# Kernel optimization log

Hardware: AMD Instinct MI355X
Metric: run time of the kernel (lower is better)

Reference implementation:

```python
import jax, jax.numpy as jnp
import numpy as np

H, HKV, D = 8, 1, 256  # query heads, kv heads, head_dim (Gemma-2B-like)


def apply_rope(x, sin, cos):
    # x: [B, h, D, S]; sin/cos: [B, 1, D//2, S]
    x1, x2 = jnp.split(x, 2, axis=-2)
    return jnp.concatenate((x1 * cos - x2 * sin, x2 * cos + x1 * sin), axis=-2)


def setup_inputs() -> dict:
    key = jax.random.key(0)
    ks = jax.random.split(key, 12)
    B, hidden, S = 2, 2048, 2048
    half = D // 2
    Xq = jax.random.normal(ks[0], (B, hidden, S), jnp.float32)
    Xkv = jax.random.normal(ks[1], (B, hidden, S), jnp.float32)
    sin_q = jax.random.uniform(ks[2], (B, 1, half, S), jnp.float32, -1.0, 1.0)
    cos_q = jax.random.uniform(ks[3], (B, 1, half, S), jnp.float32, -1.0, 1.0)
    sin_k = jax.random.uniform(ks[4], (B, 1, half, S), jnp.float32, -1.0, 1.0)
    cos_k = jax.random.uniform(ks[5], (B, 1, half, S), jnp.float32, -1.0, 1.0)
    attn_mask = jnp.zeros((B, 1, S, S), jnp.float32)
    scale = 0.02
    Wq = jax.random.normal(ks[6], (H * D, hidden), jnp.float32) * scale
    Wk = jax.random.normal(ks[7], (HKV * D, hidden), jnp.float32) * scale
    Wv = jax.random.normal(ks[8], (HKV * D, hidden), jnp.float32) * scale
    Wo = jax.random.normal(ks[9], (hidden, H * D), jnp.float32) * scale
    return {"Xq": Xq, "Xkv": Xkv, "sin_q": sin_q, "cos_q": cos_q,
            "sin_k": sin_k, "cos_k": cos_k, "attn_mask": attn_mask,
            "Wq": Wq, "Wk": Wk, "Wv": Wv, "Wo": Wo}


def reference(Xq, Xkv, sin_q, cos_q, sin_k, cos_k, attn_mask, Wq, Wk, Wv, Wo):
    B, hidden, Sq = Xq.shape
    Sk = Xkv.shape[-1]
    # ANEDenseGeneral = 1x1 conv over channels-first layout
    q = jnp.einsum('oc,bcs->bos', Wq, Xq).reshape(B, H, D, Sq)
    q = apply_rope(q, sin_q, cos_q)
    k = jnp.einsum('oc,bcs->bos', Wk, Xkv).reshape(B, HKV, D, Sk)
    k = apply_rope(k, sin_k, cos_k)
    v = jnp.einsum('oc,bcs->bos', Wv, Xkv).reshape(B, HKV, D, Sk)
    # GQA: broadcast kv heads to query heads
    rep = H // HKV
    k = jnp.repeat(k, rep, axis=1)
    v = jnp.repeat(v, rep, axis=1)
    scale = 1.0 / jnp.sqrt(jnp.asarray(D, Xq.dtype))
    scores = jnp.einsum('bhdq,bhdk->bhqk', q, k) * scale + attn_mask
    probs = jax.nn.softmax(scores, axis=-1)
    out = jnp.einsum('bhqk,bhdk->bhdq', probs, v).reshape(B, H * D, Sq)
    return jnp.einsum('oc,bcs->bos', Wo, out).astype(Xq.dtype)
```

## Files before the change

### kernel.cpp

```cpp
#include <hip/hip_runtime.h>

typedef __bf16 bf16;
typedef __bf16 bf16x8 __attribute__((ext_vector_type(8)));
typedef __bf16 bf16x4 __attribute__((ext_vector_type(4)));
typedef float f32x4 __attribute__((ext_vector_type(4)));

static constexpr int Hh = 8;
static constexpr int Dd = 256;
static constexpr int Ss = 2048;
static constexpr int Cc = 2048;
static constexpr int NS = 4096;

typedef const __attribute__((address_space(1))) unsigned int as1_u32;
typedef __attribute__((address_space(3))) unsigned int as3_u32;

__device__ __forceinline__ void gl_lds16(const void* g, void* l) {
  __builtin_amdgcn_global_load_lds((as1_u32*)(unsigned long long)g,
                                   (as3_u32*)(unsigned int)(unsigned long long)l,
                                   16, 0, 0);
}

__device__ __forceinline__ f32x4 mfma16(bf16x8 a, bf16x8 b, f32x4 c) {
  return __builtin_amdgcn_mfma_f32_16x16x32_bf16(a, b, c, 0, 0, 0);
}

__global__ __launch_bounds__(256) void cvt_all(
    const float* __restrict__ Wq, const float* __restrict__ Wo,
    const float* __restrict__ Wk, const float* __restrict__ Wv,
    bf16* __restrict__ Wq_bf, bf16* __restrict__ Wo_bf,
    bf16* __restrict__ Wkv_bf) {
  const int blk = blockIdx.x;
  const float* in;
  bf16* out;
  int base;
  if (blk < 4096) {
    in = Wq; out = Wq_bf; base = blk;
  } else if (blk < 8192) {
    in = Wo; out = Wo_bf; base = blk - 4096;
  } else if (blk < 8704) {
    in = Wk; out = Wkv_bf; base = blk - 8192;
  } else {
    in = Wv; out = Wkv_bf + (long)Dd * Cc; base = blk - 8704;
  }
  int i = (base * 256 + threadIdx.x) * 4;
  const float4 v = *(const float4*)(in + i);
  bf16x4 o;
  o[0] = (bf16)v.x; o[1] = (bf16)v.y; o[2] = (bf16)v.z; o[3] = (bf16)v.w;
  *(bf16x4*)(out + i) = o;
}

__global__ __launch_bounds__(256) void transpose_cvt(const float* __restrict__ in,
                                                     bf16* __restrict__ out,
                                                     int R, int S) {
  __shared__ float t[32][33];
  const int b = blockIdx.z;
  const long base = (long)b * R * S;
  const int s0 = blockIdx.x * 32, r0 = blockIdx.y * 32;
  const int tx = threadIdx.x, ty = threadIdx.y;
#pragma unroll
  for (int i = 0; i < 32; i += 8)
    t[ty + i][tx] = in[base + (long)(r0 + ty + i) * S + s0 + tx];
  __syncthreads();
#pragma unroll
  for (int i = 0; i < 32; i += 8)
    out[base + (long)(s0 + ty + i) * R + r0 + tx] = (bf16)t[tx][ty + i];
}

__global__ __launch_bounds__(256) void transpose_cvt4(
    const float* __restrict__ s0, const float* __restrict__ s1,
    const float* __restrict__ s2, const float* __restrict__ s3,
    bf16* __restrict__ d0, bf16* __restrict__ d1, bf16* __restrict__ d2,
    bf16* __restrict__ d3, int R, int S) {
  __shared__ float t[32][33];
  const int arr = blockIdx.y >> 2;
  const int r0 = (blockIdx.y & 3) * 32;
  const float* in = (arr == 0) ? s0 : (arr == 1) ? s1 : (arr == 2) ? s2 : s3;
  bf16* out = (arr == 0) ? d0 : (arr == 1) ? d1 : (arr == 2) ? d2 : d3;
  const int b = blockIdx.z;
  const long base = (long)b * R * S;
  const int s0i = blockIdx.x * 32;
  const int tx = threadIdx.x, ty = threadIdx.y;
#pragma unroll
  for (int i = 0; i < 32; i += 8)
    t[ty + i][tx] = in[base + (long)(r0 + ty + i) * S + s0i + tx];
  __syncthreads();
#pragma unroll
  for (int i = 0; i < 32; i += 8)
    out[base + (long)(s0i + ty + i) * R + r0 + tx] = (bf16)t[tx][ty + i];
}

__global__ __launch_bounds__(256) void rope_transpose(
    const bf16* __restrict__ qin, const bf16* __restrict__ kin,
    const bf16* __restrict__ sin_qt, const bf16* __restrict__ cos_qt,
    const bf16* __restrict__ sin_kt, const bf16* __restrict__ cos_kt,
    bf16* __restrict__ qr, bf16* __restrict__ kr) {
  __shared__ __align__(16) bf16 ti[32][264];
  const int b = blockIdx.z, y = blockIdx.y, s0 = blockIdx.x * 32;
  const bool isk = (y == 8);
  const int h = isk ? 0 : y;
  const bf16* xin = isk ? kin : qin;
  const bf16* sint = isk ? sin_kt : sin_qt;
  const bf16* cost = isk ? cos_kt : cos_qt;
  const int nH = isk ? 1 : Hh;
  bf16* xout = isk ? kr : qr;
  const int tx = threadIdx.x, ty = threadIdx.y;
  const bf16* src = xin + (long)b * Ss + (long)h * Dd * NS + s0;
#pragma unroll
  for (int i = 0; i < 32; ++i) {
    int d = ty + i * 8;
    ti[tx][d] = src[(long)d * NS + tx];
  }
  __syncthreads();
  const int t = ty * 32 + tx;
  const int s = t >> 3;
  const int dpart = t & 7;
  const bf16* sp = sint + ((long)b * Ss + s0 + s) * 128;
  const bf16* cp = cost + ((long)b * Ss + s0 + s) * 128;
  bf16* dst = xout + (((long)(b * nH + h)) * Ss + s0 + s) * Dd;
#pragma unroll
  for (int i = 0; i < 4; ++i) {
    int d0 = dpart * 8 + i * 64;
    int dh = d0 & 127;
    bf16x8 a = *(const bf16x8*)&ti[s][d0];
    bf16x8 p = *(const bf16x8*)&ti[s][(d0 < 128) ? d0 + 128 : d0 - 128];
    bf16x8 sn = *(const bf16x8*)&sp[dh];
    bf16x8 cs = *(const bf16x8*)&cp[dh];
    bf16x8 o;
#pragma unroll
    for (int j = 0; j < 8; ++j) {
      float av = (float)a[j], pv = (float)p[j];
      float c = (float)cs[j], sv = (float)sn[j];
      float val = (d0 < 128) ? (av * c - pv * sv) : (av * c + pv * sv);
      o[j] = (bf16)val;
    }
    *(bf16x8*)&dst[d0] = o;
  }
}

__global__ __launch_bounds__(256, 2) void gemm_bt(
    const bf16* __restrict__ A, const bf16* __restrict__ Bt,
    bf16* __restrict__ Cb, float* __restrict__ Cf, int M, int N, int K,
    int ntiles) {
  __shared__ __align__(16) bf16 lA[2][128 * 64];
  __shared__ __align__(16) bf16 lB[2][128 * 64];
  const int nwg = gridDim.x;
  const int cpx = nwg >> 3;
  const int bid2 = (blockIdx.x & 7) * cpx + (blockIdx.x >> 3);
  const int mt = (bid2 / ntiles) * 128, nt = (bid2 % ntiles) * 128;
  const int tid = threadIdx.x;
  const int wid = tid >> 6, lane = tid & 63;
  const int g = lane >> 4, r = lane & 15;
  const int wr = wid >> 1, wc = wid & 1;

  auto stage = [&](int buf, int kt) {
#pragma unroll
    for (int it = 0; it < 4; ++it) {
      int off = it * 4096 + tid * 16;
      int row = off >> 7;
      int c = (off >> 4) & 7;
      int csw = c ^ (row & 7);
      gl_lds16((const char*)(A + (long)(mt + row) * K + kt) + csw * 16,
               (char*)lA[buf] + it * 4096 + wid * 1024);
      gl_lds16((const char*)(Bt + (long)(nt + row) * K + kt) + csw * 16,
               (char*)lB[buf] + it * 4096 + wid * 1024);
    }
  };

  const f32x4 zf = {0.f, 0.f, 0.f, 0.f};
  f32x4 acc[4][4];
#pragma unroll
  for (int m = 0; m < 4; ++m)
#pragma unroll
    for (int n = 0; n < 4; ++n) acc[m][n] = zf;

  stage(0, 0);
  __syncthreads();
  int cur = 0;
  for (int kt = 0; kt < K; kt += 64) {
    if (kt + 64 < K) stage(cur ^ 1, kt + 64);
#pragma unroll
    for (int kk = 0; kk < 2; ++kk) {
      bf16x8 af[4], bfv[4];
#pragma unroll
      for (int m = 0; m < 4; ++m) {
        int row = wr * 64 + m * 16 + r;
        int csw = (kk * 4 + g) ^ (row & 7);
        af[m] = *(const bf16x8*)((const char*)lA[cur] + row * 128 + csw * 16);
      }
#pragma unroll
      for (int n = 0; n < 4; ++n) {
        int row = wc * 64 + n * 16 + r;
        int csw = (kk * 4 + g) ^ (row & 7);
        bfv[n] = *(const bf16x8*)((const char*)lB[cur] + row * 128 + csw * 16);
      }
#pragma unroll
      for (int m = 0; m < 4; ++m)
#pragma unroll
        for (int n = 0; n < 4; ++n)
          acc[m][n] = mfma16(af[m], bfv[n], acc[m][n]);
    }
    __syncthreads();
    cur ^= 1;
  }

#pragma unroll
  for (int m = 0; m < 4; ++m)
#pragma unroll
    for (int n = 0; n < 4; ++n)
#pragma unroll
      for (int e = 0; e < 4; ++e) {
        int orow = mt + wr * 64 + m * 16 + g * 4 + e;
        int col = nt + wc * 64 + n * 16 + r;
        if (Cf) {
          long idx = (long)(col >> 11) * ((long)Cc * Ss) + (long)orow * Ss +
                     (col & 2047);
          Cf[idx] = acc[m][n][e];
        } else {
          Cb[(long)orow * N + col] = (bf16)acc[m][n][e];
        }
      }
}

__global__ __launch_bounds__(256, 3) void gemm_bt64(
    const bf16* __restrict__ A, const bf16* __restrict__ Bt,
    bf16* __restrict__ Cb, int M, int N, int K, int ntiles) {
  __shared__ __align__(16) bf16 lA[2][64 * 64];
  __shared__ __align__(16) bf16 lB[2][128 * 64];
  const int nwg = gridDim.x;
  const int cpx = nwg >> 3;
  const int bid2 = (blockIdx.x & 7) * cpx + (blockIdx.x >> 3);
  const int mt = (bid2 / ntiles) * 64, nt = (bid2 % ntiles) * 128;
  const int tid = threadIdx.x;
  const int wid = tid >> 6, lane = tid & 63;
  const int g = lane >> 4, r = lane & 15;
  const int wn = wid;

  auto stage = [&](int buf, int kt) {
#pragma unroll
    for (int it = 0; it < 2; ++it) {
      int off = it * 4096 + tid * 16;
      int row = off >> 7;
      int c = (off >> 4) & 7;
      int csw = c ^ (row & 7);
      gl_lds16((const char*)(A + (long)(mt + row) * K + kt) + csw * 16,
               (char*)lA[buf] + it * 4096 + wid * 1024);
    }
#pragma unroll
    for (int it = 0; it < 4; ++it) {
      int off = it * 4096 + tid * 16;
      int row = off >> 7;
      int c = (off >> 4) & 7;
      int csw = c ^ (row & 7);
      gl_lds16((const char*)(Bt + (long)(nt + row) * K + kt) + csw * 16,
               (char*)lB[buf] + it * 4096 + wid * 1024);
    }
  };

  const f32x4 zf = {0.f, 0.f, 0.f, 0.f};
  f32x4 acc[4][2];
#pragma unroll
  for (int m = 0; m < 4; ++m)
#pragma unroll
    for (int n = 0; n < 2; ++n) acc[m][n] = zf;

  stage(0, 0);
  __syncthreads();
  int cur = 0;
  for (int kt = 0; kt < K; kt += 64) {
    if (kt + 64 < K) stage(cur ^ 1, kt + 64);
#pragma unroll
    for (int kk = 0; kk < 2; ++kk) {
      bf16x8 af[4], bfv[2];
#pragma unroll
      for (int m = 0; m < 4; ++m) {
        int row = m * 16 + r;
        int csw = (kk * 4 + g) ^ (row & 7);
        af[m] = *(const bf16x8*)((const char*)lA[cur] + row * 128 + csw * 16);
      }
#pragma unroll
      for (int n = 0; n < 2; ++n) {
        int row = wn * 32 + n * 16 + r;
        int csw = (kk * 4 + g) ^ (row & 7);
        bfv[n] = *(const bf16x8*)((const char*)lB[cur] + row * 128 + csw * 16);
      }
#pragma unroll
      for (int m = 0; m < 4; ++m)
#pragma unroll
        for (int n = 0; n < 2; ++n)
          acc[m][n] = mfma16(af[m], bfv[n], acc[m][n]);
    }
    __syncthreads();
    cur ^= 1;
  }

#pragma unroll
  for (int m = 0; m < 4; ++m)
#pragma unroll
    for (int n = 0; n < 2; ++n)
#pragma unroll
      for (int e = 0; e < 4; ++e) {
        int orow = mt + m * 16 + g * 4 + e;
        int col = nt + wn * 32 + n * 16 + r;
        Cb[(long)orow * N + col] = (bf16)acc[m][n][e];
      }
}

__global__ __launch_bounds__(256, 2) void attn_kernel(
    const bf16* __restrict__ qr, const bf16* __restrict__ kr,
    const bf16* __restrict__ kv, const float* __restrict__ mask,
    bf16* __restrict__ aout) {
  __shared__ __align__(16) bf16 lK[2][32 * 256];
  __shared__ __align__(16) bf16 lV[2][256 * 32];
  __shared__ __align__(16) bf16 lP[4][16 * 40];
  const int b = blockIdx.z, hg = blockIdx.y;
  const int q0 = blockIdx.x * 16;
  const int tid = threadIdx.x;
  const int wid = tid >> 6, lane = tid & 63;
  const int g = lane >> 4, q = lane & 15;
  const int h = hg * 4 + wid;

  bf16x8 qf[8];
  const bf16* qp = qr + (((long)(b * Hh + h)) * Ss + q0 + q) * Dd;
#pragma unroll
  for (int kk = 0; kk < 8; ++kk) qf[kk] = *(const bf16x8*)&qp[kk * 32 + g * 8];

  const f32x4 zf = {0.f, 0.f, 0.f, 0.f};
  f32x4 oacc[16];
#pragma unroll
  for (int i = 0; i < 16; ++i) oacc[i] = zf;
  float mrun = -3e38f, lrun = 0.f;

  const char* kb = (const char*)(kr + (long)b * Ss * Dd);
  const char* vb = (const char*)(kv + (long)256 * NS + (long)b * Ss);
  const float* mb = mask + (long)b * Ss * Ss;

  auto stage = [&](int buf, int kt) {
    const char* gK = kb + (long)kt * 512;
#pragma unroll
    for (int it = 0; it < 4; ++it) {
      int off = it * 4096 + tid * 16;
      int row = off >> 9;
      int c = (off >> 4) & 31;
      int csw = c ^ (row & 7);
      gl_lds16(gK + row * 512 + csw * 16,
               (char*)lK[buf] + it * 4096 + wid * 1024);
    }
#pragma unroll
    for (int it = 0; it < 4; ++it) {
      int off = it * 4096 + tid * 16;
      int row = off >> 6;
      int c = (off >> 4) & 3;
      int csw = c ^ ((row >> 1) & 3);
      gl_lds16(vb + (long)row * (NS * 2) + (long)kt * 2 + csw * 16,
               (char*)lV[buf] + it * 4096 + wid * 1024);
    }
  };

  stage(0, 0);
  __syncthreads();
  int cur = 0;

  for (int kt = 0; kt < Ss; kt += 32) {
    if (kt + 32 < Ss) stage(cur ^ 1, kt + 32);

    const float* mrow = mb + (long)(q0 + q) * Ss + kt;
    const float4 mv0 = *(const float4*)(mrow + 4 * g);
    const float4 mv1 = *(const float4*)(mrow + 16 + 4 * g);

    f32x4 sacc[2] = {zf, zf};
    __builtin_amdgcn_s_setprio(1);
#pragma unroll
    for (int kk = 0; kk < 8; ++kk) {
#pragma unroll
      for (int n = 0; n < 2; ++n) {
        int row = n * 16 + q;
        int csw = (kk * 4 + g) ^ (row & 7);
        bf16x8 kf = *(const bf16x8*)((const char*)lK[cur] + row * 512 + csw * 16);
        sacc[n] = mfma16(kf, qf[kk], sacc[n]);
      }
    }
    __builtin_amdgcn_s_setprio(0);

    float x[8];
    x[0] = sacc[0][0] * 0.0625f + mv0.x;
    x[1] = sacc[0][1] * 0.0625f + mv0.y;
    x[2] = sacc[0][2] * 0.0625f + mv0.z;
    x[3] = sacc[0][3] * 0.0625f + mv0.w;
    x[4] = sacc[1][0] * 0.0625f + mv1.x;
    x[5] = sacc[1][1] * 0.0625f + mv1.y;
    x[6] = sacc[1][2] * 0.0625f + mv1.z;
    x[7] = sacc[1][3] * 0.0625f + mv1.w;
    float mx = fmaxf(fmaxf(fmaxf(x[0], x[1]), fmaxf(x[2], x[3])),
                     fmaxf(fmaxf(x[4], x[5]), fmaxf(x[6], x[7])));
    mx = fmaxf(mx, __shfl_xor(mx, 16, 64));
    mx = fmaxf(mx, __shfl_xor(mx, 32, 64));
    if (mx > mrun + 8.0f) {
      float al = __expf(mrun - mx);
      lrun *= al;
#pragma unroll
      for (int nf = 0; nf < 16; ++nf) oacc[nf] *= al;
      mrun = mx;
    }
    float p[8];
    float rs = 0.f;
#pragma unroll
    for (int i = 0; i < 8; ++i) {
      p[i] = __expf(x[i] - mrun);
      rs += p[i];
    }
    rs += __shfl_xor(rs, 16, 64);
    rs += __shfl_xor(rs, 32, 64);
    lrun += rs;

    bf16x4 w0, w1;
#pragma unroll
    for (int e = 0; e < 4; ++e) { w0[e] = (bf16)p[e]; w1[e] = (bf16)p[4 + e]; }
    *(bf16x4*)&lP[wid][q * 40 + 4 * g] = w0;
    *(bf16x4*)&lP[wid][q * 40 + 16 + 4 * g] = w1;

    bf16x8 pf = *(const bf16x8*)&lP[wid][q * 40 + g * 8];
    __builtin_amdgcn_s_setprio(1);
#pragma unroll
    for (int nf = 0; nf < 16; ++nf) {
      int row = nf * 16 + q;
      int csw = g ^ ((row >> 1) & 3);
      bf16x8 vf = *(const bf16x8*)((const char*)lV[cur] + row * 64 + csw * 16);
      oacc[nf] = mfma16(vf, pf, oacc[nf]);
    }
    __builtin_amdgcn_s_setprio(0);

    __syncthreads();
    cur ^= 1;
  }

  const float inv = 1.f / lrun;
  bf16* op = aout + ((long)(b * Ss + q0 + q)) * (Hh * Dd) + h * Dd + g * 4;
#pragma unroll
  for (int nf = 0; nf < 16; ++nf) {
    bf16x4 o4;
#pragma unroll
    for (int e = 0; e < 4; ++e) o4[e] = (bf16)(oacc[nf][e] * inv);
    *(bf16x4*)&op[nf * 16] = o4;
  }
}

extern "C" void kernel_launch(void* const* d_in, const int* in_sizes, int n_in,
                              void* d_out, int out_size, void* d_ws,
                              size_t ws_size, hipStream_t stream) {
  const float* Xq = (const float*)d_in[0];
  const float* Xkv = (const float*)d_in[1];
  const float* sin_q = (const float*)d_in[2];
  const float* cos_q = (const float*)d_in[3];
  const float* sin_k = (const float*)d_in[4];
  const float* cos_k = (const float*)d_in[5];
  const float* mask = (const float*)d_in[6];
  const float* Wq = (const float*)d_in[7];
  const float* Wk = (const float*)d_in[8];
  const float* Wv = (const float*)d_in[9];
  const float* Wo = (const float*)d_in[10];
  float* out = (float*)d_out;

  char* ws = (char*)d_ws;
  const size_t MB = 1u << 20;
  bf16* Wq_bf = (bf16*)(ws + 0 * MB);
  bf16* Wo_bf = (bf16*)(ws + 8 * MB);
  bf16* Wkv_bf = (bf16*)(ws + 16 * MB);
  bf16* sin_qt = (bf16*)(ws + 18 * MB);
  bf16* cos_qt = (bf16*)(ws + 19 * MB);
  bf16* sin_kt = (bf16*)(ws + 20 * MB);
  bf16* cos_kt = (bf16*)(ws + 21 * MB);
  bf16* Xtq = (bf16*)(ws + 22 * MB);
  bf16* Xtkv = (bf16*)(ws + 38 * MB);
  bf16* q_tmp = (bf16*)(ws + 54 * MB);
  bf16* kv_tmp = (bf16*)(ws + 70 * MB);
  bf16* qr = (bf16*)(ws + 22 * MB);
  bf16* kr = (bf16*)(ws + 38 * MB);
  bf16* attnb = (bf16*)(ws + 54 * MB);

  dim3 b256(256), b32x8(32, 8);

  cvt_all<<<dim3(9216), b256, 0, stream>>>(Wq, Wo, Wk, Wv, Wq_bf, Wo_bf,
                                           Wkv_bf);

  transpose_cvt<<<dim3(64, 64, 2), b32x8, 0, stream>>>(Xq, Xtq, Cc, Ss);
  transpose_cvt<<<dim3(64, 64, 2), b32x8, 0, stream>>>(Xkv, Xtkv, Cc, Ss);
  transpose_cvt4<<<dim3(64, 16, 2), b32x8, 0, stream>>>(
      sin_q, cos_q, sin_k, cos_k, sin_qt, cos_qt, sin_kt, cos_kt, 128, Ss);

  gemm_bt<<<dim3(512), b256, 0, stream>>>(Wq_bf, Xtq, q_tmp, nullptr,
                                          Cc, NS, Cc, NS / 128);
  gemm_bt64<<<dim3(256), b256, 0, stream>>>(Wkv_bf, Xtkv, kv_tmp,
                                            2 * Dd, NS, Cc, NS / 128);

  rope_transpose<<<dim3(64, 9, 2), b32x8, 0, stream>>>(
      q_tmp, kv_tmp, sin_qt, cos_qt, sin_kt, cos_kt, qr, kr);

  attn_kernel<<<dim3(128, 2, 2), b256, 0, stream>>>(qr, kr, kv_tmp, mask,
                                                    attnb);

  gemm_bt<<<dim3(512), b256, 0, stream>>>(Wo_bf, attnb, nullptr, out,
                                          Cc, NS, Cc, NS / 128);
}
```

Baseline: 266.8 us.

## Split attention over two KV halves with merge kernel and single-buffered V

Attention work is split along the key dimension into two halves, doubling the grid to 1024 blocks. Partial outputs plus running max and sum go to scratch (the output buffer is reused for the partials), and a new merge kernel combines them. V staging drops to a single buffer with an extra barrier to cut LDS and allow 3 blocks per CU, and block indices are remapped for locality. This trades more parallelism and occupancy against extra partial-output traffic, a second launch and more synchronisation in the inner loop.

```diff
diff --git a/kernel.cpp b/kernel.cpp
--- a/kernel.cpp
+++ b/kernel.cpp
@@ -305,15 +305,20 @@
       }
 }
 
-__global__ __launch_bounds__(256, 2) void attn_kernel(
+__global__ __launch_bounds__(256, 3) void attn_split(
     const bf16* __restrict__ qr, const bf16* __restrict__ kr,
     const bf16* __restrict__ kv, const float* __restrict__ mask,
-    bf16* __restrict__ aout) {
+    bf16* __restrict__ opart, float2* __restrict__ ml) {
   __shared__ __align__(16) bf16 lK[2][32 * 256];
-  __shared__ __align__(16) bf16 lV[2][256 * 32];
+  __shared__ __align__(16) bf16 lV[256 * 32];
   __shared__ __align__(16) bf16 lP[4][16 * 40];
-  const int b = blockIdx.z, hg = blockIdx.y;
-  const int q0 = blockIdx.x * 16;
+  const int i = blockIdx.x;
+  const int flat = (i & 7) * 128 + (i >> 3);
+  const int b = flat >> 9;
+  const int rem = flat & 511;
+  const int kvh = rem >> 8;
+  const int hg = (rem >> 7) & 1;
+  const int q0 = (rem & 127) * 16;
   const int tid = threadIdx.x;
   const int wid = tid >> 6, lane = tid & 63;
   const int g = lane >> 4, q = lane & 15;
@@ -327,14 +332,14 @@
   const f32x4 zf = {0.f, 0.f, 0.f, 0.f};
   f32x4 oacc[16];
 #pragma unroll
-  for (int i = 0; i < 16; ++i) oacc[i] = zf;
+  for (int i2 = 0; i2 < 16; ++i2) oacc[i2] = zf;
   float mrun = -3e38f, lrun = 0.f;
 
   const char* kb = (const char*)(kr + (long)b * Ss * Dd);
   const char* vb = (const char*)(kv + (long)256 * NS + (long)b * Ss);
   const float* mb = mask + (long)b * Ss * Ss;
 
-  auto stage = [&](int buf, int kt) {
+  auto stageK = [&](int buf, int kt) {
     const char* gK = kb + (long)kt * 512;
 #pragma unroll
     for (int it = 0; it < 4; ++it) {
@@ -345,6 +350,8 @@
       gl_lds16(gK + row * 512 + csw * 16,
                (char*)lK[buf] + it * 4096 + wid * 1024);
     }
+  };
+  auto stageV = [&](int kt) {
 #pragma unroll
     for (int it = 0; it < 4; ++it) {
       int off = it * 4096 + tid * 16;
@@ -352,16 +359,18 @@
       int c = (off >> 4) & 3;
       int csw = c ^ ((row >> 1) & 3);
       gl_lds16(vb + (long)row * (NS * 2) + (long)kt * 2 + csw * 16,
-               (char*)lV[buf] + it * 4096 + wid * 1024);
+               (char*)lV + it * 4096 + wid * 1024);
     }
   };
 
-  stage(0, 0);
+  const int kbeg = kvh * (Ss / 2), kend = kbeg + (Ss / 2);
+  stageK(0, kbeg);
+  stageV(kbeg);
   __syncthreads();
   int cur = 0;
 
-  for (int kt = 0; kt < Ss; kt += 32) {
-    if (kt + 32 < Ss) stage(cur ^ 1, kt + 32);
+  for (int kt = kbeg; kt < kend; kt += 32) {
+    if (kt + 32 < kend) stageK(cur ^ 1, kt + 32);
 
     const float* mrow = mb + (long)(q0 + q) * Ss + kt;
     const float4 mv0 = *(const float4*)(mrow + 4 * g);
@@ -404,9 +413,9 @@
     float p[8];
     float rs = 0.f;
 #pragma unroll
-    for (int i = 0; i < 8; ++i) {
-      p[i] = __expf(x[i] - mrun);
-      rs += p[i];
+    for (int i2 = 0; i2 < 8; ++i2) {
+      p[i2] = __expf(x[i2] - mrun);
+      rs += p[i2];
     }
     rs += __shfl_xor(rs, 16, 64);
     rs += __shfl_xor(rs, 32, 64);
@@ -418,29 +427,72 @@
     *(bf16x4*)&lP[wid][q * 40 + 4 * g] = w0;
     *(bf16x4*)&lP[wid][q * 40 + 16 + 4 * g] = w1;
 
+    __syncthreads();
+
     bf16x8 pf = *(const bf16x8*)&lP[wid][q * 40 + g * 8];
     __builtin_amdgcn_s_setprio(1);
 #pragma unroll
     for (int nf = 0; nf < 16; ++nf) {
       int row = nf * 16 + q;
       int csw = g ^ ((row >> 1) & 3);
-      bf16x8 vf = *(const bf16x8*)((const char*)lV[cur] + row * 64 + csw * 16);
+      bf16x8 vf = *(const bf16x8*)((const char*)lV + row * 64 + csw * 16);
       oacc[nf] = mfma16(vf, pf, oacc[nf]);
     }
     __builtin_amdgcn_s_setprio(0);
 
     __syncthreads();
+    if (kt + 32 < kend) stageV(kt + 32);
     cur ^= 1;
   }
 
   const float inv = 1.f / lrun;
-  bf16* op = aout + ((long)(b * Ss + q0 + q)) * (Hh * Dd) + h * Dd + g * 4;
+  const long ridx = (((long)(b * 2 + kvh) * Hh + h)) * Ss + q0 + q;
+  bf16* po = opart + ridx * Dd + g * 4;
 #pragma unroll
   for (int nf = 0; nf < 16; ++nf) {
     bf16x4 o4;
 #pragma unroll
     for (int e = 0; e < 4; ++e) o4[e] = (bf16)(oacc[nf][e] * inv);
-    *(bf16x4*)&op[nf * 16] = o4;
+    *(bf16x4*)&po[nf * 16] = o4;
+  }
+  if (g == 0) {
+    float2 v;
+    v.x = mrun;
+    v.y = lrun;
+    ml[ridx] = v;
+  }
+}
+
+__global__ __launch_bounds__(256) void attn_merge(
+    const bf16* __restrict__ opart, const float2* __restrict__ ml,
+    bf16* __restrict__ attnb) {
+  const long t = (long)blockIdx.x * 256 + threadIdx.x;
+  const int d0 = (int)(t & 7) << 5;
+  const long R = t >> 3;
+  const long b = R >> 14;
+  const long rem = R & 16383;
+  const int h = (int)(rem >> 11);
+  const int s = (int)(rem & 2047);
+  const long i0 = (b * 2 + 0) * ((long)Hh * Ss) + rem;
+  const long i1 = (b * 2 + 1) * ((long)Hh * Ss) + rem;
+  const float2 ml0 = ml[i0], ml1 = ml[i1];
+  const float m = fmaxf(ml0.x, ml1.x);
+  const float w0 = ml0.y * __expf(ml0.x - m);
+  const float w1 = ml1.y * __expf(ml1.x - m);
+  const float inv = 1.f / (w0 + w1);
+  const float s0 = w0 * inv, s1 = w1 * inv;
+  const bf16* p0 = opart + i0 * Dd + d0;
+  const bf16* p1 = opart + i1 * Dd + d0;
+  bf16* po = attnb + ((long)b * Ss + s) * (Hh * Dd) + h * Dd + d0;
+#pragma unroll
+  for (int j = 0; j < 4; ++j) {
+    bf16x8 v0 = *(const bf16x8*)(p0 + j * 8);
+    bf16x8 v1 = *(const bf16x8*)(p1 + j * 8);
+    bf16x8 o;
+#pragma unroll
+    for (int e = 0; e < 8; ++e)
+      o[e] = (bf16)((float)v0[e] * s0 + (float)v1[e] * s1);
+    *(bf16x8*)(po + j * 8) = o;
   }
 }
 
@@ -471,11 +523,13 @@
   bf16* cos_kt = (bf16*)(ws + 21 * MB);
   bf16* Xtq = (bf16*)(ws + 22 * MB);
   bf16* Xtkv = (bf16*)(ws + 38 * MB);
+  float2* ml = (float2*)(ws + 44 * MB);
   bf16* q_tmp = (bf16*)(ws + 54 * MB);
   bf16* kv_tmp = (bf16*)(ws + 70 * MB);
   bf16* qr = (bf16*)(ws + 22 * MB);
   bf16* kr = (bf16*)(ws + 38 * MB);
   bf16* attnb = (bf16*)(ws + 54 * MB);
+  bf16* opart = (bf16*)d_out;
 
   dim3 b256(256), b32x8(32, 8);
 
@@ -495,8 +549,8 @@
   rope_transpose<<<dim3(64, 9, 2), b32x8, 0, stream>>>(
       q_tmp, kv_tmp, sin_qt, cos_qt, sin_kt, cos_kt, qr, kr);
 
-  attn_kernel<<<dim3(128, 2, 2), b256, 0, stream>>>(qr, kr, kv_tmp, mask,
-                                                    attnb);
+  attn_split<<<dim3(1024), b256, 0, stream>>>(qr, kr, kv_tmp, mask, opart, ml);
+  attn_merge<<<dim3(1024), b256, 0, stream>>>(opart, ml, attnb);
 
   gemm_bt<<<dim3(512), b256, 0, stream>>>(Wo_bf, attnb, nullptr, out,
                                           Cc, NS, Cc, NS / 128);
```

Result: slower. 282.0 us (+5.7%).
